# Kernel tuning notes

Measured on AMD Instinct MI355X. Metric: run time of the kernel, lower is better.

Reference implementation:

```python
import jax, jax.numpy as jnp
import numpy as np

HIDDEN = 1024
NUM_HEADS = 16
HEAD_DIM = HIDDEN // NUM_HEADS


def setup_inputs() -> dict:
    key = jax.random.key(0)
    ks = jax.random.split(key, 10)
    B, T, S = 2, 2048, 2048
    sc = 1.0 / np.sqrt(HIDDEN)
    inp = {
        "tgt": jax.random.normal(ks[0], (B, T, HIDDEN), jnp.float32),
        "src": jax.random.normal(ks[1], (B, S, HIDDEN), jnp.float32),
        # per-head projection weights stacked: [H, in_dim, head_dim]
        "Wq": jax.random.normal(ks[2], (NUM_HEADS, HIDDEN, HEAD_DIM), jnp.float32) * sc,
        "bq": jnp.zeros((NUM_HEADS, HEAD_DIM), jnp.float32),
        "Wk": jax.random.normal(ks[3], (NUM_HEADS, HIDDEN, HEAD_DIM), jnp.float32) * sc,
        "bk": jnp.zeros((NUM_HEADS, HEAD_DIM), jnp.float32),
        "Wv": jax.random.normal(ks[4], (NUM_HEADS, HIDDEN, HEAD_DIM), jnp.float32) * sc,
        "bv": jnp.zeros((NUM_HEADS, HEAD_DIM), jnp.float32),
        "Wo": jax.random.normal(ks[5], (HIDDEN, HIDDEN), jnp.float32) * sc,
        "bo": jnp.zeros((HIDDEN,), jnp.float32),
    }
    return inp


def reference(tgt, src, Wq, bq, Wk, bk, Wv, bv, Wo, bo):
    # Per-head linear projections (vectorized over heads)
    q = jnp.einsum("btd,hdk->bhtk", tgt, Wq) + bq[None, :, None, :]  # [B,H,T,Dh]
    k = jnp.einsum("bsd,hdk->bhsk", src, Wk) + bk[None, :, None, :]  # [B,H,S,Dh]
    v = jnp.einsum("bsd,hdk->bhsk", src, Wv) + bv[None, :, None, :]  # [B,H,S,Dh]
    scale = 1.0 / jnp.sqrt(jnp.asarray(HEAD_DIM, q.dtype))
    scores = jnp.einsum("bhtk,bhsk->bhts", q, k) * scale  # [B,H,T,S]
    weights = jax.nn.softmax(scores, axis=-1)
    out = jnp.einsum("bhts,bhsk->bhtk", weights, v)  # [B,H,T,Dh]
    # concat heads along last dim (head order matches torch cat)
    B, H, T, Dh = out.shape
    h = out.transpose(0, 2, 1, 3).reshape(B, T, H * Dh)
    return h @ Wo + bo
```

## Files before the change

### kernel.cpp

```cpp
#include <hip/hip_runtime.h>

typedef _Float16 f16;
typedef __attribute__((ext_vector_type(4))) _Float16 f16x4;
typedef __attribute__((ext_vector_type(8))) _Float16 f16x8;
typedef __attribute__((ext_vector_type(4))) float f32x4;

constexpr int HID = 1024, NH = 16, DH = 64, BB = 2, TT = 2048, SS = 2048;
constexpr float SCL = 0.18033688011112042f;

__device__ __forceinline__ void gl_lds16(const void* g, void* l) {
  __builtin_amdgcn_global_load_lds(
      (const __attribute__((address_space(1))) void*)g,
      (__attribute__((address_space(3))) void*)l, 16, 0, 0);
}

#define VMCNT(N) asm volatile("s_waitcnt vmcnt(" #N ")" ::: "memory")

#if __has_builtin(__builtin_amdgcn_exp2f)
#define EXP2(x) __builtin_amdgcn_exp2f(x)
#else
#define EXP2(x) exp2f(x)
#endif

__global__ __launch_bounds__(256) void k_cvt_act(const float* __restrict__ in,
                                                 f16* __restrict__ out, int n) {
  int i = (blockIdx.x * 256 + threadIdx.x) * 4;
  if (i < n) {
    float4 v = *(const float4*)(in + i);
    f16x4 o; o[0] = (f16)v.x; o[1] = (f16)v.y; o[2] = (f16)v.z; o[3] = (f16)v.w;
    *(f16x4*)(out + i) = o;
  }
}

__global__ __launch_bounds__(256) void k_cvt_w(const float* __restrict__ in,
                                               f16* __restrict__ out, int C,
                                               float scale) {
  __shared__ f16 t[64 * 72];
  int c0 = blockIdx.x * 64, d0 = blockIdx.y * 64, slab = blockIdx.z;
  const float* ip = in + (size_t)slab * 1024 * C;
  int tid = threadIdx.x;
  int r = tid >> 4, cq = (tid & 15) * 4;
  for (int rr = 0; rr < 64; rr += 16) {
    float4 v = *(const float4*)(ip + (size_t)(d0 + r + rr) * C + (c0 + cq));
    t[(cq + 0) * 72 + r + rr] = (f16)(v.x * scale);
    t[(cq + 1) * 72 + r + rr] = (f16)(v.y * scale);
    t[(cq + 2) * 72 + r + rr] = (f16)(v.z * scale);
    t[(cq + 3) * 72 + r + rr] = (f16)(v.w * scale);
  }
  __syncthreads();
  int c = tid >> 2, dq = (tid & 3) * 16;
  f16* op = out + (size_t)(slab * C + c0 + c) * 1024 + d0 + dq;
  *(f16x8*)op = *(const f16x8*)&t[c * 72 + dq];
  *(f16x8*)(op + 8) = *(const f16x8*)&t[c * 72 + dq + 8];
}

template <int MODE>
__global__ __launch_bounds__(256) void k_gemm(const f16* __restrict__ A,
                                              const f16* __restrict__ Bt,
                                              const float* __restrict__ bias,
                                              float bscale,
                                              void* __restrict__ outp) {
  __shared__ f16 lA[3][128 * 64];
  __shared__ f16 lB[3][128 * 64];
  const int tid = threadIdx.x;
  const int lane = tid & 63, hi = lane >> 4, t16 = lane & 15;
  const int w = tid >> 6;
  const int wr = (w >> 1) * 64, wc = (w & 1) * 64;
  const int id = blockIdx.y * 8 + blockIdx.x;
  const int m0 = ((id & 7) * 4 + ((id >> 3) & 3)) * 128;
  const int n0 = (id >> 5) * 128;

  f32x4 acc[4][4];
#pragma unroll
  for (int i = 0; i < 4; i++)
#pragma unroll
    for (int j = 0; j < 4; j++) acc[i][j] = (f32x4){0.f, 0.f, 0.f, 0.f};

  auto STAGE = [&](int s, int kt) {
#pragma unroll
    for (int it = 0; it < 4; ++it) {
      int u = it * 256 + tid, row = u >> 3, un = u & 7;
      int gc = kt * 64 + ((un ^ (row & 7)) << 3);
      gl_lds16(A + (size_t)(m0 + row) * 1024 + gc, (char*)&lA[s][0] + u * 16);
    }
#pragma unroll
    for (int it = 0; it < 4; ++it) {
      int u = it * 256 + tid, row = u >> 3, un = u & 7;
      int gc = kt * 64 + ((un ^ (row & 7)) << 3);
      gl_lds16(Bt + (size_t)(n0 + row) * 1024 + gc, (char*)&lB[s][0] + u * 16);
    }
  };

  STAGE(0, 0);
  STAGE(1, 1);
  int cs = 0;
  for (int kt = 0; kt < 16; ++kt) {
    if (kt < 15) { VMCNT(8); } else { VMCNT(0); }
    __builtin_amdgcn_s_barrier();
    __builtin_amdgcn_sched_barrier(0);
    int ns = cs + 2; if (ns >= 3) ns -= 3;
    if (kt + 2 < 16) STAGE(ns, kt + 2);
#pragma unroll
    for (int ks = 0; ks < 2; ++ks) {
      f16x8 af[4], bf[4];
#pragma unroll
      for (int mi = 0; mi < 4; mi++) {
        int r = wr + mi * 16 + t16;
        af[mi] = *(const f16x8*)&lA[cs][r * 64 + (((ks * 4 + hi) ^ (r & 7)) << 3)];
      }
#pragma unroll
      for (int ni = 0; ni < 4; ni++) {
        int r = wc + ni * 16 + t16;
        bf[ni] = *(const f16x8*)&lB[cs][r * 64 + (((ks * 4 + hi) ^ (r & 7)) << 3)];
      }
      __builtin_amdgcn_s_setprio(1);
#pragma unroll
      for (int mi = 0; mi < 4; mi++)
#pragma unroll
        for (int ni = 0; ni < 4; ni++)
          acc[mi][ni] = __builtin_amdgcn_mfma_f32_16x16x32_f16(
              af[mi], bf[ni], acc[mi][ni], 0, 0, 0);
      __builtin_amdgcn_s_setprio(0);
    }
    cs = (cs == 2) ? 0 : cs + 1;
  }

#pragma unroll
  for (int mi = 0; mi < 4; mi++) {
#pragma unroll
    for (int ni = 0; ni < 4; ni++) {
#pragma unroll
      for (int rg = 0; rg < 4; rg++) {
        int m = m0 + wr + mi * 16 + hi * 4 + rg;
        int n = n0 + wc + ni * 16 + t16;
        float v = acc[mi][ni][rg] + bias[n] * bscale;
        if (MODE == 0) {
          ((f16*)outp)[(size_t)m * 1024 + n] = (f16)v;
        } else if (MODE == 1) {
          int b = m >> 11, s = m & 2047;
          ((f16*)outp)[(((size_t)(b * NH + (n >> 6)) * DH + (n & 63)) << 11) + s] = (f16)v;
        } else {
          ((float*)outp)[(size_t)m * 1024 + n] = v;
        }
      }
    }
  }
}

__global__ __launch_bounds__(256) void k_attn(const f16* __restrict__ Q,
                                              const f16* __restrict__ K,
                                              const f16* __restrict__ Vt,
                                              f16* __restrict__ Hout) {
  __shared__ f16 lK[3][64 * 64];
  __shared__ f16 lV[3][64 * 64];
  const int tid = threadIdx.x;
  const int lane = tid & 63, hi = lane >> 4, t16 = lane & 15;
  const int w = tid >> 6;
  const int id = blockIdx.y * 16 + blockIdx.x;
  const int bh = (id & 7) * 4 + ((id >> 3) & 3);
  const int b = bh >> 4, h = bh & 15;
  const int tq = (id >> 5) * 128 + w * 32;

  f16x8 qa[2][2];
#pragma unroll
  for (int g = 0; g < 2; ++g)
#pragma unroll
    for (int ks = 0; ks < 2; ++ks)
      qa[g][ks] = *(const f16x8*)(Q + (size_t)(b * TT + tq + g * 16 + t16) * HID +
                                  h * DH + ks * 32 + hi * 8);
#pragma unroll
  for (int g = 0; g < 2; ++g)
#pragma unroll
    for (int ks = 0; ks < 2; ++ks) asm volatile("" : "+v"(qa[g][ks]));

  float lrow[2] = {0.f, 0.f};
  f32x4 o[2][4];
#pragma unroll
  for (int g = 0; g < 2; ++g)
#pragma unroll
    for (int dc = 0; dc < 4; ++dc) o[g][dc] = (f32x4){0.f, 0.f, 0.f, 0.f};

  auto STAGE = [&](int s, int sb) {
#pragma unroll
    for (int it = 0; it < 2; ++it) {
      int u = it * 256 + tid, row = u >> 3, un = u & 7;
      int kc = (un ^ (row & 7)) << 3;
      gl_lds16(K + (size_t)(b * SS + sb * 64 + row) * HID + h * DH + kc,
               (char*)&lK[s][0] + u * 16);
      gl_lds16(Vt + ((size_t)(b * NH + h) * DH + row) * SS + sb * 64 + kc,
               (char*)&lV[s][0] + u * 16);
    }
  };

  STAGE(0, 0);
  STAGE(1, 1);
  int cs = 0;
  for (int i = 0; i < 32; ++i) {
    if (i < 31) { VMCNT(4); } else { VMCNT(0); }
    __builtin_amdgcn_s_barrier();
    __builtin_amdgcn_sched_barrier(0);
    int ns = cs + 2; if (ns >= 3) ns -= 3;
    if (i + 2 < 32) STAGE(ns, i + 2);

    f16x8 kb[4][2];
#pragma unroll
    for (int sb = 0; sb < 4; ++sb) {
      int r = sb * 16 + t16;
#pragma unroll
      for (int ks = 0; ks < 2; ++ks)
        kb[sb][ks] = *(const f16x8*)&lK[cs][r * 64 + (((ks * 4 + hi) ^ (r & 7)) << 3)];
    }
    f32x4 sc[4][2];
#pragma unroll
    for (int sb = 0; sb < 4; ++sb)
#pragma unroll
      for (int g = 0; g < 2; ++g) sc[sb][g] = (f32x4){0.f, 0.f, 0.f, 0.f};
    __builtin_amdgcn_s_setprio(1);
#pragma unroll
    for (int sb = 0; sb < 4; ++sb)
#pragma unroll
      for (int g = 0; g < 2; ++g)
#pragma unroll
        for (int ks = 0; ks < 2; ++ks)
          sc[sb][g] = __builtin_amdgcn_mfma_f32_16x16x32_f16(
              kb[sb][ks], qa[g][ks], sc[sb][g], 0, 0, 0);
    __builtin_amdgcn_s_setprio(0);

    f16x4 pf[2][4];
#pragma unroll
    for (int g = 0; g < 2; ++g) {
#pragma unroll
      for (int sb = 0; sb < 4; ++sb) {
        float p0 = EXP2(sc[sb][g][0]);
        float p1 = EXP2(sc[sb][g][1]);
        float p2 = EXP2(sc[sb][g][2]);
        float p3 = EXP2(sc[sb][g][3]);
        lrow[g] += (p0 + p1) + (p2 + p3);
        f16x4 pv; pv[0] = (f16)p0; pv[1] = (f16)p1; pv[2] = (f16)p2; pv[3] = (f16)p3;
        pf[g][sb] = pv;
      }
    }

    f16x4 vf[4][4];
#pragma unroll
    for (int dc = 0; dc < 4; ++dc) {
#pragma unroll
      for (int sk = 0; sk < 4; ++sk) {
        int chunk = ((2 * sk + (hi >> 1)) ^ (t16 & 7));
        vf[dc][sk] = *(const f16x4*)&lV[cs][(dc * 16 + t16) * 64 + chunk * 8 + (hi & 1) * 4];
      }
    }

    __builtin_amdgcn_s_setprio(1);
#pragma unroll
    for (int g = 0; g < 2; ++g)
#pragma unroll
      for (int dc = 0; dc < 4; ++dc)
#pragma unroll
        for (int sk = 0; sk < 4; ++sk)
          o[g][dc] = __builtin_amdgcn_mfma_f32_16x16x16f16(vf[dc][sk], pf[g][sk],
                                                           o[g][dc], 0, 0, 0);
    __builtin_amdgcn_s_setprio(0);

    cs = (cs == 2) ? 0 : cs + 1;
  }

#pragma unroll
  for (int g = 0; g < 2; ++g) {
    float l = lrow[g];
    l += __shfl_xor(l, 16);
    l += __shfl_xor(l, 32);
    float rinv = 1.0f / l;
#pragma unroll
    for (int dc = 0; dc < 4; ++dc) {
      f16x4 ov;
#pragma unroll
      for (int rg = 0; rg < 4; ++rg) ov[rg] = (f16)(o[g][dc][rg] * rinv);
      *(f16x4*)(Hout + (size_t)(b * TT + tq + g * 16 + t16) * HID + h * DH +
                dc * 16 + hi * 4) = ov;
    }
  }
}

extern "C" void kernel_launch(void* const* d_in, const int* in_sizes, int n_in,
                              void* d_out, int out_size, void* d_ws, size_t ws_size,
                              hipStream_t stream) {
  const float* tgt = (const float*)d_in[0];
  const float* src = (const float*)d_in[1];
  const float* Wq = (const float*)d_in[2];
  const float* bq = (const float*)d_in[3];
  const float* Wk = (const float*)d_in[4];
  const float* bk = (const float*)d_in[5];
  const float* Wv = (const float*)d_in[6];
  const float* bv = (const float*)d_in[7];
  const float* Wo = (const float*)d_in[8];
  const float* bo = (const float*)d_in[9];
  float* out = (float*)d_out;

  char* ws = (char*)d_ws;
  f16* tgt16 = (f16*)(ws);
  f16* src16 = (f16*)(ws + (8u << 20));
  f16* wq16 = (f16*)(ws + (16u << 20));
  f16* wk16 = (f16*)(ws + (18u << 20));
  f16* wv16 = (f16*)(ws + (20u << 20));
  f16* wo16 = (f16*)(ws + (22u << 20));
  f16* Q16 = (f16*)(ws + (24u << 20));
  f16* K16 = (f16*)(ws + (32u << 20));
  f16* Vt16 = (f16*)(ws + (40u << 20));
  f16* h16 = (f16*)(ws + (48u << 20));

  k_cvt_act<<<4096, 256, 0, stream>>>(tgt, tgt16, BB * TT * HID);
  k_cvt_act<<<4096, 256, 0, stream>>>(src, src16, BB * SS * HID);
  k_cvt_w<<<dim3(1, 16, 16), 256, 0, stream>>>(Wq, wq16, 64, SCL);
  k_cvt_w<<<dim3(1, 16, 16), 256, 0, stream>>>(Wk, wk16, 64, 1.0f);
  k_cvt_w<<<dim3(1, 16, 16), 256, 0, stream>>>(Wv, wv16, 64, 1.0f);
  k_cvt_w<<<dim3(16, 16, 1), 256, 0, stream>>>(Wo, wo16, 1024, 1.0f);

  k_gemm<0><<<dim3(8, 32), 256, 0, stream>>>(tgt16, wq16, bq, SCL, Q16);
  k_gemm<0><<<dim3(8, 32), 256, 0, stream>>>(src16, wk16, bk, 1.0f, K16);
  k_gemm<1><<<dim3(8, 32), 256, 0, stream>>>(src16, wv16, bv, 1.0f, Vt16);

  k_attn<<<dim3(16, 32), 256, 0, stream>>>(Q16, K16, Vt16, h16);

  k_gemm<2><<<dim3(8, 32), 256, 0, stream>>>(h16, wo16, bo, 1.0f, out);
}
```

Measured before the change: 240.2 us.

## Merge QKV GEMMs into one launch, single-buffer LDS, halve output GEMM tile

Replaces the three separate Q/K/V projection launches with one 768-block kernel that picks operands per block, so the GPU sees one wave of work instead of three 256-block launches. The triple-buffered async LDS pipeline is replaced by a single buffer with __syncthreads. That cuts LDS use, which may allow more resident blocks per CU, but loads no longer overlap compute. The output projection uses 128x64 tiles and 512 blocks to improve CU coverage, at the cost of more A-tile reloads.

```diff
diff --git a/kernel.cpp b/kernel.cpp
--- a/kernel.cpp
+++ b/kernel.cpp
@@ -54,64 +54,55 @@
   *(f16x8*)(op + 8) = *(const f16x8*)&t[c * 72 + dq + 8];
 }
 
-template <int MODE>
-__global__ __launch_bounds__(256) void k_gemm(const f16* __restrict__ A,
-                                              const f16* __restrict__ Bt,
-                                              const float* __restrict__ bias,
-                                              float bscale,
-                                              void* __restrict__ outp) {
-  __shared__ f16 lA[3][128 * 64];
-  __shared__ f16 lB[3][128 * 64];
+__global__ __launch_bounds__(256) void k_gemm_qkv(
+    const f16* __restrict__ tgt16, const f16* __restrict__ src16,
+    const f16* __restrict__ wq, const f16* __restrict__ wk,
+    const f16* __restrict__ wv, const float* __restrict__ bq,
+    const float* __restrict__ bk, const float* __restrict__ bv,
+    f16* __restrict__ Qo, f16* __restrict__ Ko, f16* __restrict__ Vo) {
+  __shared__ f16 lA[128 * 64];
+  __shared__ f16 lB[128 * 64];
   const int tid = threadIdx.x;
   const int lane = tid & 63, hi = lane >> 4, t16 = lane & 15;
   const int w = tid >> 6;
   const int wr = (w >> 1) * 64, wc = (w & 1) * 64;
-  const int id = blockIdx.y * 8 + blockIdx.x;
-  const int m0 = ((id & 7) * 4 + ((id >> 3) & 3)) * 128;
-  const int n0 = (id >> 5) * 128;
+  const int i = blockIdx.x;
+  const int xcd = i & 7, j = i >> 3;
+  const int z = j % 3;
+  const int r = j / 3;
+  const int m0 = (xcd * 4 + (r & 3)) * 128, n0 = (r >> 2) * 128;
+  const f16* A = z ? src16 : tgt16;
+  const f16* Bt = (z == 0) ? wq : ((z == 1) ? wk : wv);
+  const float* bias = (z == 0) ? bq : ((z == 1) ? bk : bv);
+  const float bscale = (z == 0) ? SCL : 1.0f;
 
   f32x4 acc[4][4];
 #pragma unroll
-  for (int i = 0; i < 4; i++)
-#pragma unroll
-    for (int j = 0; j < 4; j++) acc[i][j] = (f32x4){0.f, 0.f, 0.f, 0.f};
-
-  auto STAGE = [&](int s, int kt) {
+  for (int a = 0; a < 4; a++)
+#pragma unroll
+    for (int bq_ = 0; bq_ < 4; bq_++) acc[a][bq_] = (f32x4){0.f, 0.f, 0.f, 0.f};
+
+  for (int kt = 0; kt < 16; ++kt) {
 #pragma unroll
     for (int it = 0; it < 4; ++it) {
       int u = it * 256 + tid, row = u >> 3, un = u & 7;
       int gc = kt * 64 + ((un ^ (row & 7)) << 3);
-      gl_lds16(A + (size_t)(m0 + row) * 1024 + gc, (char*)&lA[s][0] + u * 16);
-    }
-#pragma unroll
-    for (int it = 0; it < 4; ++it) {
-      int u = it * 256 + tid, row = u >> 3, un = u & 7;
-      int gc = kt * 64 + ((un ^ (row & 7)) << 3);
-      gl_lds16(Bt + (size_t)(n0 + row) * 1024 + gc, (char*)&lB[s][0] + u * 16);
-    }
-  };
-
-  STAGE(0, 0);
-  STAGE(1, 1);
-  int cs = 0;
-  for (int kt = 0; kt < 16; ++kt) {
-    if (kt < 15) { VMCNT(8); } else { VMCNT(0); }
-    __builtin_amdgcn_s_barrier();
-    __builtin_amdgcn_sched_barrier(0);
-    int ns = cs + 2; if (ns >= 3) ns -= 3;
-    if (kt + 2 < 16) STAGE(ns, kt + 2);
+      gl_lds16(A + (size_t)(m0 + row) * 1024 + gc, (char*)lA + u * 16);
+      gl_lds16(Bt + (size_t)(n0 + row) * 1024 + gc, (char*)lB + u * 16);
+    }
+    __syncthreads();
 #pragma unroll
     for (int ks = 0; ks < 2; ++ks) {
       f16x8 af[4], bf[4];
 #pragma unroll
       for (int mi = 0; mi < 4; mi++) {
-        int r = wr + mi * 16 + t16;
-        af[mi] = *(const f16x8*)&lA[cs][r * 64 + (((ks * 4 + hi) ^ (r & 7)) << 3)];
+        int rr = wr + mi * 16 + t16;
+        af[mi] = *(const f16x8*)&lA[rr * 64 + (((ks * 4 + hi) ^ (rr & 7)) << 3)];
       }
 #pragma unroll
       for (int ni = 0; ni < 4; ni++) {
-        int r = wc + ni * 16 + t16;
-        bf[ni] = *(const f16x8*)&lB[cs][r * 64 + (((ks * 4 + hi) ^ (r & 7)) << 3)];
+        int rr = wc + ni * 16 + t16;
+        bf[ni] = *(const f16x8*)&lB[rr * 64 + (((ks * 4 + hi) ^ (rr & 7)) << 3)];
       }
       __builtin_amdgcn_s_setprio(1);
 #pragma unroll
@@ -122,29 +113,106 @@
               af[mi], bf[ni], acc[mi][ni], 0, 0, 0);
       __builtin_amdgcn_s_setprio(0);
     }
-    cs = (cs == 2) ? 0 : cs + 1;
-  }
-
-#pragma unroll
-  for (int mi = 0; mi < 4; mi++) {
-#pragma unroll
-    for (int ni = 0; ni < 4; ni++) {
+    __syncthreads();
+  }
+
+  if (z < 2) {
+    f16* outp = z ? Ko : Qo;
+#pragma unroll
+    for (int mi = 0; mi < 4; mi++)
+#pragma unroll
+      for (int ni = 0; ni < 4; ni++)
+#pragma unroll
+        for (int rg = 0; rg < 4; rg++) {
+          int m = m0 + wr + mi * 16 + hi * 4 + rg;
+          int n = n0 + wc + ni * 16 + t16;
+          outp[(size_t)m * 1024 + n] = (f16)(acc[mi][ni][rg] + bias[n] * bscale);
+        }
+  } else {
+#pragma unroll
+    for (int mi = 0; mi < 4; mi++)
+#pragma unroll
+      for (int ni = 0; ni < 4; ni++)
+#pragma unroll
+        for (int rg = 0; rg < 4; rg++) {
+          int m = m0 + wr + mi * 16 + hi * 4 + rg;
+          int n = n0 + wc + ni * 16 + t16;
+          int b = m >> 11, s = m & 2047;
+          Vo[(((size_t)(b * NH + (n >> 6)) * DH + (n & 63)) << 11) + s] =
+              (f16)(acc[mi][ni][rg] + bias[n]);
+        }
+  }
+}
+
+__global__ __launch_bounds__(256) void k_gemm_o(const f16* __restrict__ A,
+                                                const f16* __restrict__ Bt,
+                                                const float* __restrict__ bias,
+                                                float* __restrict__ outp) {
+  __shared__ f16 lA[128 * 64];
+  __shared__ f16 lB[64 * 64];
+  const int tid = threadIdx.x;
+  const int lane = tid & 63, hi = lane >> 4, t16 = lane & 15;
+  const int w = tid >> 6;
+  const int wr = (w >> 1) * 64, wc = (w & 1) * 32;
+  const int i = blockIdx.x;
+  const int xcd = i & 7, j = i >> 3;
+  const int m0 = (xcd * 4 + (j & 3)) * 128, n0 = (j >> 2) * 64;
+
+  f32x4 acc[4][2];
+#pragma unroll
+  for (int a = 0; a < 4; a++)
+#pragma unroll
+    for (int bq_ = 0; bq_ < 2; bq_++) acc[a][bq_] = (f32x4){0.f, 0.f, 0.f, 0.f};
+
+  for (int kt = 0; kt < 16; ++kt) {
+#pragma unroll
+    for (int it = 0; it < 4; ++it) {
+      int u = it * 256 + tid, row = u >> 3, un = u & 7;
+      int gc = kt * 64 + ((un ^ (row & 7)) << 3);
+      gl_lds16(A + (size_t)(m0 + row) * 1024 + gc, (char*)lA + u * 16);
+    }
+#pragma unroll
+    for (int it = 0; it < 2; ++it) {
+      int u = it * 256 + tid, row = u >> 3, un = u & 7;
+      int gc = kt * 64 + ((un ^ (row & 7)) << 3);
+      gl_lds16(Bt + (size_t)(n0 + row) * 1024 + gc, (char*)lB + u * 16);
+    }
+    __syncthreads();
+#pragma unroll
+    for (int ks = 0; ks < 2; ++ks) {
+      f16x8 af[4], bf[2];
+#pragma unroll
+      for (int mi = 0; mi < 4; mi++) {
+        int rr = wr + mi * 16 + t16;
+        af[mi] = *(const f16x8*)&lA[rr * 64 + (((ks * 4 + hi) ^ (rr & 7)) << 3)];
+      }
+#pragma unroll
+      for (int ni = 0; ni < 2; ni++) {
+        int rr = wc + ni * 16 + t16;
+        bf[ni] = *(const f16x8*)&lB[rr * 64 + (((ks * 4 + hi) ^ (rr & 7)) << 3)];
+      }
+      __builtin_amdgcn_s_setprio(1);
+#pragma unroll
+      for (int mi = 0; mi < 4; mi++)
+#pragma unroll
+        for (int ni = 0; ni < 2; ni++)
+          acc[mi][ni] = __builtin_amdgcn_mfma_f32_16x16x32_f16(
+              af[mi], bf[ni], acc[mi][ni], 0, 0, 0);
+      __builtin_amdgcn_s_setprio(0);
+    }
+    __syncthreads();
+  }
+
+#pragma unroll
+  for (int mi = 0; mi < 4; mi++)
+#pragma unroll
+    for (int ni = 0; ni < 2; ni++)
 #pragma unroll
       for (int rg = 0; rg < 4; rg++) {
         int m = m0 + wr + mi * 16 + hi * 4 + rg;
         int n = n0 + wc + ni * 16 + t16;
-        float v = acc[mi][ni][rg] + bias[n] * bscale;
-        if (MODE == 0) {
-          ((f16*)outp)[(size_t)m * 1024 + n] = (f16)v;
-        } else if (MODE == 1) {
-          int b = m >> 11, s = m & 2047;
-          ((f16*)outp)[(((size_t)(b * NH + (n >> 6)) * DH + (n & 63)) << 11) + s] = (f16)v;
-        } else {
-          ((float*)outp)[(size_t)m * 1024 + n] = v;
-        }
-      }
-    }
-  }
+        outp[(size_t)m * 1024 + n] = acc[mi][ni][rg] + bias[n];
+      }
 }
 
 __global__ __launch_bounds__(256) void k_attn(const f16* __restrict__ Q,
@@ -316,11 +384,10 @@
   k_cvt_w<<<dim3(1, 16, 16), 256, 0, stream>>>(Wv, wv16, 64, 1.0f);
   k_cvt_w<<<dim3(16, 16, 1), 256, 0, stream>>>(Wo, wo16, 1024, 1.0f);
 
-  k_gemm<0><<<dim3(8, 32), 256, 0, stream>>>(tgt16, wq16, bq, SCL, Q16);
-  k_gemm<0><<<dim3(8, 32), 256, 0, stream>>>(src16, wk16, bk, 1.0f, K16);
-  k_gemm<1><<<dim3(8, 32), 256, 0, stream>>>(src16, wv16, bv, 1.0f, Vt16);
+  k_gemm_qkv<<<768, 256, 0, stream>>>(tgt16, src16, wq16, wk16, wv16,
+                                      bq, bk, bv, Q16, K16, Vt16);
 
   k_attn<<<dim3(16, 32), 256, 0, stream>>>(Q16, K16, Vt16, h16);
 
-  k_gemm<2><<<dim3(8, 32), 256, 0, stream>>>(h16, wo16, bo, 1.0f, out);
-}
+  k_gemm_o<<<512, 256, 0, stream>>>(h16, wo16, bo, out);
+}
```

Measured after the change: 221.9 us. 1.08x faster.
